# Kernel optimization log

Hardware: AMD Instinct MI355X
Metric: run time of the kernel (lower is better)

The kernel has to match this reference:

```python
import jax, jax.numpy as jnp
import numpy as np

KERNEL_MUL = 2.0
KERNEL_NUM = 5


def setup_inputs() -> dict:
    key = jax.random.key(0)
    k1, k2 = jax.random.split(key)
    N, D = 4096, 256
    source = jax.random.normal(k1, (N, D), dtype=jnp.float32)
    target = jax.random.normal(k2, (N, D), dtype=jnp.float32)
    return {"source": source, "target": target}


def reference(source, target):
    ns = source.shape[0]
    total = jnp.concatenate([source, target], axis=0)  # [2N, D]
    n = total.shape[0]
    # Pairwise squared L2 distance via GEMM trick (same math as expand+sub+square+sum)
    sq = jnp.sum(total * total, axis=1)               # [2N]
    gram = total @ total.T                             # [2N, 2N]
    l2 = sq[:, None] + sq[None, :] - 2.0 * gram        # [2N, 2N]
    # Bandwidth from detached distances (torch uses .data)
    l2_sg = jax.lax.stop_gradient(l2)
    bandwidth = jnp.sum(l2_sg) / (n * n - n)
    bandwidth = bandwidth / (KERNEL_MUL ** (KERNEL_NUM // 2))
    bws = bandwidth * (KERNEL_MUL ** jnp.arange(KERNEL_NUM, dtype=l2.dtype))  # [K]
    # Multi-kernel Gaussian RBF sum: sum_k exp(-l2 / bw_k)
    kernels = jnp.exp(-l2[None, :, :] / bws[:, None, None]).sum(axis=0)  # [2N, 2N]
    XX = kernels[:ns, :ns]
    YY = kernels[ns:, ns:]
    XY = kernels[:ns, ns:]
    YX = kernels[ns:, :ns]
    loss = jnp.mean(XX) + jnp.mean(YY) - jnp.mean(XY) - jnp.mean(YX)
    return loss
```

## Files before the change

kernel.cpp:

```cpp
#include <hip/hip_runtime.h>
#include <hip/hip_bf16.h>
#include <stdint.h>


#define NROW 8192
#define NS   4096
#define DD   256
#define TILE 128
#define BK   64
#define NTB  64
#define NBLK (NTB*(NTB+1)/2)
#define K1B  128

typedef __bf16 bf16_t;
typedef __bf16 bf16x8 __attribute__((ext_vector_type(8)));
typedef __bf16 bf16x4 __attribute__((ext_vector_type(4)));
typedef float  f32x4  __attribute__((ext_vector_type(4)));

#define OFF_CPAR 0
#define OFF_SQ   1024
#define OFF_CS   (OFF_SQ + 8192*4)
#define OFF_SS   (OFF_CS + K1B*256*4)
#define OFF_TBF  (1<<18)

__device__ __forceinline__ void async16(const void* g, void* l) {
  __builtin_amdgcn_global_load_lds(
      (const __attribute__((address_space(1))) void*)(uintptr_t)g,
      (__attribute__((address_space(3))) void*)(uintptr_t)l, 16, 0, 0);
}

__global__ __launch_bounds__(256) void k1_prep(const float* __restrict__ src,
                                               const float* __restrict__ tgt,
                                               float* __restrict__ sq,
                                               float* __restrict__ cs_part,
                                               float* __restrict__ ss_part,
                                               bf16_t* __restrict__ tbf,
                                               float* __restrict__ out) {
  const int b = blockIdx.x, tid = threadIdx.x;
  const int w = tid >> 6, lane = tid & 63;
  if (b == 0 && tid == 0) out[0] = 0.f;
  float4 csum = make_float4(0.f, 0.f, 0.f, 0.f);
  float wss = 0.f;
  for (int r = 0; r < 16; ++r) {
    const int row = b * 64 + w * 16 + r;
    const float* rp = (row < NS) ? (src + (size_t)row * DD)
                                 : (tgt + (size_t)(row - NS) * DD);
    float4 v = ((const float4*)rp)[lane];
    bf16x4 o;
    o[0] = (bf16_t)v.x; o[1] = (bf16_t)v.y; o[2] = (bf16_t)v.z; o[3] = (bf16_t)v.w;
    *(bf16x4*)(tbf + (size_t)row * DD + lane * 4) = o;
    float s2 = v.x*v.x + v.y*v.y + v.z*v.z + v.w*v.w;
    #pragma unroll
    for (int off = 32; off >= 1; off >>= 1) s2 += __shfl_xor(s2, off);
    if (lane == 0) { sq[row] = s2; wss += s2; }
    csum.x += v.x; csum.y += v.y; csum.z += v.z; csum.w += v.w;
  }
  __shared__ float cls[4][256];
  __shared__ float sls[4];
  ((float4*)cls[w])[lane] = csum;
  if (lane == 0) sls[w] = wss;
  __syncthreads();
  cs_part[b * 256 + tid] = cls[0][tid] + cls[1][tid] + cls[2][tid] + cls[3][tid];
  if (tid == 0) ss_part[b] = sls[0] + sls[1] + sls[2] + sls[3];
}

__global__ __launch_bounds__(256) void k2_bw(const float* __restrict__ cs_part,
                                             const float* __restrict__ ss_part,
                                             float* __restrict__ cpar) {
  const int tid = threadIdx.x, w = tid >> 6, lane = tid & 63;
  float c = 0.f;
  for (int b = 0; b < K1B; ++b) c += cs_part[b * 256 + tid];
  double csq = (double)c * (double)c;
  double ssq = (tid < K1B) ? (double)ss_part[tid] : 0.0;
  #pragma unroll
  for (int off = 32; off >= 1; off >>= 1) {
    csq += __shfl_xor(csq, off);
    ssq += __shfl_xor(ssq, off);
  }
  __shared__ double rc[4], rs[4];
  if (lane == 0) { rc[w] = csq; rs[w] = ssq; }
  __syncthreads();
  if (tid == 0) {
    double C = rc[0] + rc[1] + rc[2] + rc[3];
    double S = rs[0] + rs[1] + rs[2] + rs[3];
    const double n = (double)NROW;
    double suml2 = 2.0 * n * S - 2.0 * C;
    double bw0 = suml2 / (n * n - n) / 4.0;
    cpar[0] = (float)(1.4426950408889634 / (16.0 * bw0));
  }
}

__global__ __launch_bounds__(256) void k3_mmd(const bf16_t* __restrict__ tbf,
                                              const float* __restrict__ sqg,
                                              const float* __restrict__ cpar,
                                              float* __restrict__ out) {
  __shared__ __align__(16) bf16_t As[TILE * BK];
  __shared__ __align__(16) bf16_t Bs[TILE * BK];
  __shared__ float red[4];

  const int t = blockIdx.x;
  int bi = (int)((sqrtf(8.0f * (float)t + 1.0f) - 1.0f) * 0.5f);
  while ((bi + 1) * (bi + 2) / 2 <= t) ++bi;
  while (bi * (bi + 1) / 2 > t) --bi;
  const int bj = t - bi * (bi + 1) / 2;

  const int tid = threadIdx.x;
  const int w = tid >> 6, lane = tid & 63;
  const int m0 = (w >> 1) * 64, n0 = (w & 1) * 64;
  const int wbase = tid & ~63;

  const float cE = cpar[0];

  f32x4 acc[4][4] = {};

  const bf16_t* Ag = tbf + (size_t)bi * TILE * DD;
  const bf16_t* Bg = tbf + (size_t)bj * TILE * DD;

  for (int kt = 0; kt < 4; ++kt) {
    __syncthreads();
    #pragma unroll
    for (int it = 0; it < 4; ++it) {
      const int c   = it * 256 + tid;
      const int r   = c >> 3;
      const int kcs = (c & 7) ^ (r & 7);
      const bf16_t* asrc = Ag + (size_t)r * DD + kt * 64 + kcs * 8;
      const bf16_t* bsrc = Bg + (size_t)r * DD + kt * 64 + kcs * 8;
      char* ldst  = (char*)As + (size_t)(it * 256 + wbase) * 16;
      char* ldst2 = (char*)Bs + (size_t)(it * 256 + wbase) * 16;
      async16(asrc, ldst);
      async16(bsrc, ldst2);
    }
    __syncthreads();
    #pragma unroll
    for (int kk = 0; kk < 2; ++kk) {
      const int kc = kk * 4 + (lane >> 4);
      const int kphys = (kc ^ (lane & 7)) * 8;
      bf16x8 af[4], bfr[4];
      #pragma unroll
      for (int mi = 0; mi < 4; ++mi)
        af[mi] = *(const bf16x8*)(As + (m0 + mi * 16 + (lane & 15)) * BK + kphys);
      #pragma unroll
      for (int ni = 0; ni < 4; ++ni)
        bfr[ni] = *(const bf16x8*)(Bs + (n0 + ni * 16 + (lane & 15)) * BK + kphys);
      #pragma unroll
      for (int mi = 0; mi < 4; ++mi)
        #pragma unroll
        for (int ni = 0; ni < 4; ++ni)
          acc[mi][ni] = __builtin_amdgcn_mfma_f32_16x16x32_bf16(
              af[mi], bfr[ni], acc[mi][ni], 0, 0, 0);
    }
  }

  const float c2 = 2.0f * cE;
  float bjv[4];
  #pragma unroll
  for (int ni = 0; ni < 4; ++ni)
    bjv[ni] = sqg[bj * TILE + n0 + ni * 16 + (lane & 15)] * cE;

  float tsum = 0.f;
  #pragma unroll
  for (int mi = 0; mi < 4; ++mi) {
    float ai[4];
    #pragma unroll
    for (int r = 0; r < 4; ++r)
      ai[r] = sqg[bi * TILE + m0 + mi * 16 + (lane >> 4) * 4 + r] * cE;
    #pragma unroll
    for (int ni = 0; ni < 4; ++ni) {
      #pragma unroll
      for (int r = 0; r < 4; ++r) {
        const float g = acc[mi][ni][r];
        const float e = fmaf(g, c2, -(ai[r] + bjv[ni]));
        const float v   = __builtin_amdgcn_exp2f(e);
        const float v2  = v * v;
        const float v4  = v2 * v2;
        const float v8  = v4 * v4;
        const float v16 = v8 * v8;
        tsum += v + v2 + v4 + v8 + v16;
      }
    }
  }
  #pragma unroll
  for (int off = 32; off >= 1; off >>= 1) tsum += __shfl_xor(tsum, off);
  if (lane == 0) red[w] = tsum;
  __syncthreads();
  if (tid == 0) {
    const float s    = red[0] + red[1] + red[2] + red[3];
    const float sign = ((bi < NS / TILE) == (bj < NS / TILE)) ? 1.f : -1.f;
    const float wt   = (bi == bj) ? 1.f : 2.f;
    atomicAdd(out, s * sign * wt * (1.0f / ((float)NS * (float)NS)));
  }
}

extern "C" void kernel_launch(void* const* d_in, const int* in_sizes, int n_in,
                              void* d_out, int out_size, void* d_ws, size_t ws_size,
                              hipStream_t stream) {
  const float* src = (const float*)d_in[0];
  const float* tgt = (const float*)d_in[1];
  char* ws = (char*)d_ws;
  float*  cpar = (float*)(ws + OFF_CPAR);
  float*  sq   = (float*)(ws + OFF_SQ);
  float*  csp  = (float*)(ws + OFF_CS);
  float*  ssp  = (float*)(ws + OFF_SS);
  bf16_t* tbf  = (bf16_t*)(ws + OFF_TBF);
  float*  out  = (float*)d_out;

  k1_prep<<<K1B, 256, 0, stream>>>(src, tgt, sq, csp, ssp, tbf, out);
  k2_bw  <<<1,   256, 0, stream>>>(csp, ssp, cpar);
  k3_mmd <<<NBLK,256, 0, stream>>>(tbf, sq, cpar, out);
}
```

Before: 110.3 us.

## Enlarge MMD tiles to 256 with 512-thread blocks and packed-float epilogue

Doubles the Gram tile to 256x256 per block with 8 waves, each computing a 128x64 sub-tile, so fewer triangular blocks are launched and staged operands are reused more. The exp/kernel-sum epilogue is rewritten with 2-wide float vectors so the compiler can emit packed FP32 ops. This raises accumulator registers per wave and LDS per block, and leaves fewer blocks (528), which can cause load imbalance across CUs.

Result: no change. 110.4 us (+0.1%).

```diff
diff --git a/kernel.cpp b/kernel.cpp
--- a/kernel.cpp
+++ b/kernel.cpp
@@ -6,9 +6,9 @@
 #define NROW 8192
 #define NS   4096
 #define DD   256
-#define TILE 128
+#define TILE 256
 #define BK   64
-#define NTB  64
+#define NTB  32
 #define NBLK (NTB*(NTB+1)/2)
 #define K1B  128
 
@@ -16,6 +16,7 @@
 typedef __bf16 bf16x8 __attribute__((ext_vector_type(8)));
 typedef __bf16 bf16x4 __attribute__((ext_vector_type(4)));
 typedef float  f32x4  __attribute__((ext_vector_type(4)));
+typedef float  f32x2  __attribute__((ext_vector_type(2)));
 
 #define OFF_CPAR 0
 #define OFF_SQ   1024
@@ -90,13 +91,13 @@
   }
 }
 
-__global__ __launch_bounds__(256) void k3_mmd(const bf16_t* __restrict__ tbf,
+__global__ __launch_bounds__(512) void k3_mmd(const bf16_t* __restrict__ tbf,
                                               const float* __restrict__ sqg,
                                               const float* __restrict__ cpar,
                                               float* __restrict__ out) {
   __shared__ __align__(16) bf16_t As[TILE * BK];
   __shared__ __align__(16) bf16_t Bs[TILE * BK];
-  __shared__ float red[4];
+  __shared__ float red[8];
 
   const int t = blockIdx.x;
   int bi = (int)((sqrtf(8.0f * (float)t + 1.0f) - 1.0f) * 0.5f);
@@ -106,12 +107,13 @@
 
   const int tid = threadIdx.x;
   const int w = tid >> 6, lane = tid & 63;
-  const int m0 = (w >> 1) * 64, n0 = (w & 1) * 64;
+  const int m0 = (w >> 2) * 128;
+  const int n0 = (w & 3) * 64;
   const int wbase = tid & ~63;
 
   const float cE = cpar[0];
 
-  f32x4 acc[4][4] = {};
+  f32x4 acc[8][4] = {};
 
   const bf16_t* Ag = tbf + (size_t)bi * TILE * DD;
   const bf16_t* Bg = tbf + (size_t)bj * TILE * DD;
@@ -120,30 +122,28 @@
     __syncthreads();
     #pragma unroll
     for (int it = 0; it < 4; ++it) {
-      const int c   = it * 256 + tid;
+      const int c   = it * 512 + tid;
       const int r   = c >> 3;
       const int kcs = (c & 7) ^ (r & 7);
-      const bf16_t* asrc = Ag + (size_t)r * DD + kt * 64 + kcs * 8;
-      const bf16_t* bsrc = Bg + (size_t)r * DD + kt * 64 + kcs * 8;
-      char* ldst  = (char*)As + (size_t)(it * 256 + wbase) * 16;
-      char* ldst2 = (char*)Bs + (size_t)(it * 256 + wbase) * 16;
-      async16(asrc, ldst);
-      async16(bsrc, ldst2);
+      async16(Ag + (size_t)r * DD + kt * 64 + kcs * 8,
+              (char*)As + (size_t)(it * 512 + wbase) * 16);
+      async16(Bg + (size_t)r * DD + kt * 64 + kcs * 8,
+              (char*)Bs + (size_t)(it * 512 + wbase) * 16);
     }
     __syncthreads();
     #pragma unroll
     for (int kk = 0; kk < 2; ++kk) {
       const int kc = kk * 4 + (lane >> 4);
       const int kphys = (kc ^ (lane & 7)) * 8;
-      bf16x8 af[4], bfr[4];
-      #pragma unroll
-      for (int mi = 0; mi < 4; ++mi)
+      bf16x8 af[8], bfr[4];
+      #pragma unroll
+      for (int mi = 0; mi < 8; ++mi)
         af[mi] = *(const bf16x8*)(As + (m0 + mi * 16 + (lane & 15)) * BK + kphys);
       #pragma unroll
       for (int ni = 0; ni < 4; ++ni)
         bfr[ni] = *(const bf16x8*)(Bs + (n0 + ni * 16 + (lane & 15)) * BK + kphys);
       #pragma unroll
-      for (int mi = 0; mi < 4; ++mi)
+      for (int mi = 0; mi < 8; ++mi)
         #pragma unroll
         for (int ni = 0; ni < 4; ++ni)
           acc[mi][ni] = __builtin_amdgcn_mfma_f32_16x16x32_bf16(
@@ -151,40 +151,44 @@
     }
   }
 
-  const float c2 = 2.0f * cE;
-  float bjv[4];
-  #pragma unroll
-  for (int ni = 0; ni < 4; ++ni)
-    bjv[ni] = sqg[bj * TILE + n0 + ni * 16 + (lane & 15)] * cE;
-
-  float tsum = 0.f;
-  #pragma unroll
-  for (int mi = 0; mi < 4; ++mi) {
-    float ai[4];
-    #pragma unroll
-    for (int r = 0; r < 4; ++r)
-      ai[r] = sqg[bi * TILE + m0 + mi * 16 + (lane >> 4) * 4 + r] * cE;
+  const f32x2 c2 = {2.0f * cE, 2.0f * cE};
+  f32x2 bj2[4];
+  #pragma unroll
+  for (int ni = 0; ni < 4; ++ni) {
+    const float b = sqg[bj * TILE + n0 + ni * 16 + (lane & 15)] * cE;
+    bj2[ni][0] = b; bj2[ni][1] = b;
+  }
+
+  f32x2 t2 = {0.f, 0.f};
+  #pragma unroll
+  for (int mi = 0; mi < 8; ++mi) {
+    const int mbase = bi * TILE + m0 + mi * 16 + (lane >> 4) * 4;
+    f32x2 ai2[2];
+    ai2[0][0] = sqg[mbase + 0] * cE; ai2[0][1] = sqg[mbase + 1] * cE;
+    ai2[1][0] = sqg[mbase + 2] * cE; ai2[1][1] = sqg[mbase + 3] * cE;
     #pragma unroll
     for (int ni = 0; ni < 4; ++ni) {
       #pragma unroll
-      for (int r = 0; r < 4; ++r) {
-        const float g = acc[mi][ni][r];
-        const float e = fmaf(g, c2, -(ai[r] + bjv[ni]));
-        const float v   = __builtin_amdgcn_exp2f(e);
-        const float v2  = v * v;
-        const float v4  = v2 * v2;
-        const float v8  = v4 * v4;
-        const float v16 = v8 * v8;
-        tsum += v + v2 + v4 + v8 + v16;
+      for (int h = 0; h < 2; ++h) {
+        f32x2 g; g[0] = acc[mi][ni][2*h]; g[1] = acc[mi][ni][2*h+1];
+        f32x2 e = g * c2 - (ai2[h] + bj2[ni]);
+        f32x2 v;
+        v[0] = __builtin_amdgcn_exp2f(e[0]);
+        v[1] = __builtin_amdgcn_exp2f(e[1]);
+        f32x2 v2 = v * v, v4 = v2 * v2, v8 = v4 * v4, v16 = v8 * v8;
+        t2 += ((v + v2) + (v4 + v8)) + v16;
       }
     }
   }
+  float tsum = t2[0] + t2[1];
   #pragma unroll
   for (int off = 32; off >= 1; off >>= 1) tsum += __shfl_xor(tsum, off);
   if (lane == 0) red[w] = tsum;
   __syncthreads();
   if (tid == 0) {
-    const float s    = red[0] + red[1] + red[2] + red[3];
+    float s = 0.f;
+    #pragma unroll
+    for (int i = 0; i < 8; ++i) s += red[i];
     const float sign = ((bi < NS / TILE) == (bj < NS / TILE)) ? 1.f : -1.f;
     const float wt   = (bi == bj) ? 1.f : 2.f;
     atomicAdd(out, s * sign * wt * (1.0f / ((float)NS * (float)NS)));
@@ -206,5 +210,5 @@
 
   k1_prep<<<K1B, 256, 0, stream>>>(src, tgt, sq, csp, ssp, tbf, out);
   k2_bw  <<<1,   256, 0, stream>>>(csp, ssp, cpar);
-  k3_mmd <<<NBLK,256, 0, stream>>>(tbf, sq, cpar, out);
-}
+  k3_mmd <<<NBLK,512, 0, stream>>>(tbf, sq, cpar, out);
+}
```
